# Performance work log

Measured on AMD Instinct MI355X. Metric: run time of the kernel, lower is better.

## Reference

```python
import jax, jax.numpy as jnp
import numpy as np

N_NODES = 40000
N_EDGES = 1280000
D_FEAT = 1024
HIDDEN = 64
N_CLASSES = 40


def gcn_conv(x, edge_index, W, b):
    # PyG GCNConv: linear transform, add self-loops, symmetric deg^{-1/2} normalization, scatter-add
    n = x.shape[0]
    h = x @ W  # [N, out]
    loop = jnp.arange(n, dtype=edge_index.dtype)
    row = jnp.concatenate([edge_index[0], loop])  # source
    col = jnp.concatenate([edge_index[1], loop])  # target
    deg = jax.ops.segment_sum(jnp.ones_like(col, dtype=x.dtype), col, num_segments=n)
    dinv = jnp.where(deg > 0, jax.lax.rsqrt(deg), 0.0).astype(x.dtype)
    norm = dinv[row] * dinv[col]  # [E+N]
    msg = h[row] * norm[:, None]
    out = jax.ops.segment_sum(msg, col, num_segments=n)
    return out + b


def setup_inputs() -> dict:
    key = jax.random.key(0)
    k1, k2, k3, k4 = jax.random.split(key, 4)
    x = jax.random.normal(k1, (N_NODES, D_FEAT), dtype=jnp.float32)
    edge_index = jax.random.randint(k2, (2, N_EDGES), 0, N_NODES, dtype=jnp.int32)
    W1 = jax.random.normal(k3, (D_FEAT, HIDDEN), dtype=jnp.float32) * (1.0 / np.sqrt(D_FEAT))
    b1 = jnp.zeros((HIDDEN,), dtype=jnp.float32)
    W2 = jax.random.normal(k4, (HIDDEN, N_CLASSES), dtype=jnp.float32) * (1.0 / np.sqrt(HIDDEN))
    b2 = jnp.zeros((N_CLASSES,), dtype=jnp.float32)
    return {"x": x, "edge_index": edge_index, "W1": W1, "b1": b1, "W2": W2, "b2": b2}


def reference(x, edge_index, W1, b1, W2, b2):
    h = gcn_conv(x, edge_index, W1, b1)
    h = jax.nn.relu(h)
    # F.dropout(training=False) -> identity in eval mode
    h = gcn_conv(h, edge_index, W2, b2)
    return jax.nn.log_softmax(h, axis=1)
```

## Files before the change

### kernel.cpp

```cpp
#include <hip/hip_runtime.h>
#include <hip/hip_bf16.h>
#include <math.h>

#define N_NODES 40000
#define N_EDGES 1280000
#define D_FEAT 1024
#define HIDDEN 64
#define N_CLASSES 40
#define NB 157
#define CHUNK 2048
#define SORT_STAGE 10240

typedef _Float16 f16x8 __attribute__((ext_vector_type(8)));
typedef float f32x4 __attribute__((ext_vector_type(4)));

__device__ __forceinline__ int wscan64(int v, int lane) {
#pragma unroll
    for (int d = 1; d < 64; d <<= 1) {
        int t = __shfl_up(v, d, 64);
        v += (lane >= d) ? t : 0;
    }
    return v;
}


#define HIST_BLOCKS 313
#define CONV_BLOCKS 256

__global__ __launch_bounds__(256) void k_pre(const int* __restrict__ col,
                                             int* __restrict__ btot,
                                             const float* __restrict__ W,
                                             _Float16* __restrict__ Wt) {
    __shared__ int h[NB];
    int tid = threadIdx.x;
    if (blockIdx.x < HIST_BLOCKS) {
        if (tid < NB) h[tid] = 0;
        __syncthreads();
        int e0 = blockIdx.x * 4096;
#pragma unroll
        for (int t = 0; t < 4; ++t) {
            int e = e0 + t * 1024 + tid * 4;
            if (e < N_EDGES) {
                int4 c = *(const int4*)&col[e];
                atomicAdd(&h[c.x >> 8], 1);
                atomicAdd(&h[c.y >> 8], 1);
                atomicAdd(&h[c.z >> 8], 1);
                atomicAdd(&h[c.w >> 8], 1);
            }
        }
        __syncthreads();
        if (tid < NB && h[tid]) atomicAdd(&btot[tid], h[tid]);
    } else {
        int i = (blockIdx.x - HIST_BLOCKS) * 256 + tid;
        int n = i & 63, k = i >> 6;
        Wt[n * D_FEAT + k] = (_Float16)W[k * HIDDEN + n];
    }
}


__global__ __launch_bounds__(256) void k_scanbb(const int* __restrict__ btot,
                                                int* __restrict__ bb) {
    __shared__ int wsum[4];
    const int tid = threadIdx.x;
    const int wave = tid >> 6, lane = tid & 63;
    int v = (tid < NB) ? btot[tid] : 0;
    int iv = wscan64(v, lane);
    if (lane == 63) wsum[wave] = iv;
    __syncthreads();
    int add = 0;
#pragma unroll
    for (int w = 0; w < 3; ++w)
        add += (w < wave) ? wsum[w] : 0;
    if (tid < NB) bb[tid] = iv + add - v;
}


__global__ __launch_bounds__(256) void k_binscatter(const int* __restrict__ row,
                                                    const int* __restrict__ col,
                                                    const int* __restrict__ bb,
                                                    int* __restrict__ gcur,
                                                    unsigned* __restrict__ sedge) {
    __shared__ unsigned stage[CHUNK];
    __shared__ unsigned char bo[CHUNK];
    __shared__ int hist[NB];
    __shared__ int lo[NB];
    __shared__ int cur[NB];
    __shared__ int dst[NB];
    __shared__ int wsum[4];
    const int tid = threadIdx.x;
    const int wave = tid >> 6, lane = tid & 63;
    const int e0 = blockIdx.x * CHUNK;

    if (tid < NB) { hist[tid] = 0; cur[tid] = 0; }
    __syncthreads();

    int c[8];
#pragma unroll
    for (int t = 0; t < 8; ++t) {
        int e = tid + t * 256;
        c[t] = col[e0 + e];
        atomicAdd(&hist[c[t] >> 8], 1);
    }
    __syncthreads();

    int hv = (tid < NB) ? hist[tid] : 0;
    int iv = wscan64(hv, lane);
    if (lane == 63) wsum[wave] = iv;
    __syncthreads();
    int add = 0;
#pragma unroll
    for (int w = 0; w < 3; ++w)
        add += (w < wave) ? wsum[w] : 0;
    if (tid < NB) {
        int excl = iv + add - hv;
        lo[tid] = excl;
        int cp = hv ? atomicAdd(&gcur[tid], hv) : 0;
        dst[tid] = bb[tid] + cp - excl;
    }
    __syncthreads();

#pragma unroll
    for (int t = 0; t < 8; ++t) {
        int e = tid + t * 256;
        int b = c[t] >> 8;
        int p = lo[b] + atomicAdd(&cur[b], 1);
        stage[p] = ((unsigned)(c[t] & 255) << 16) | (unsigned)row[e0 + e];
        bo[p] = (unsigned char)b;
    }
    __syncthreads();
    for (int i = tid; i < CHUNK; i += 256)
        sedge[dst[bo[i]] + i] = stage[i];
}


__global__ __launch_bounds__(512) void k_bucketsort(const unsigned* __restrict__ sedge,
                                                    const int* __restrict__ btot,
                                                    const int* __restrict__ bb,
                                                    int* __restrict__ off,
                                                    float* __restrict__ dinv,
                                                    unsigned short* __restrict__ sorted) {
    __shared__ int hist[256];
    __shared__ int cur[256];
    __shared__ unsigned short st[SORT_STAGE];
    __shared__ int wsum[4];
    const int tid = threadIdx.x;
    const int wave = tid >> 6, lane = tid & 63;
    const int b = blockIdx.x;
    const int base = bb[b];
    const int cnt  = btot[b];
    const int end  = base + cnt;

    if (tid < 256) hist[tid] = 0;
    __syncthreads();

    for (int i = base + tid; i < end; i += 512)
        atomicAdd(&hist[sedge[i] >> 16], 1);
    __syncthreads();

    int v = 0, iv = 0;
    if (tid < 256) {
        v = hist[tid];
        iv = wscan64(v, lane);
        if (lane == 63) wsum[wave] = iv;
    }
    __syncthreads();
    if (tid < 256) {
        int add = 0;
#pragma unroll
        for (int w = 0; w < 3; ++w)
            add += (w < wave) ? wsum[w] : 0;
        int excl = iv + add - v;
        cur[tid] = excl;
        int col0 = b << 8;
        int ncol = min(256, N_NODES - col0);
        if (tid < ncol) {
            off[col0 + tid] = base + excl;
            dinv[col0 + tid] = rsqrtf((float)(v + 1));
        }
    }
    if (b == NB - 1 && tid == 0) off[N_NODES] = N_EDGES;
    __syncthreads();

    if (cnt <= SORT_STAGE) {
        for (int i = base + tid; i < end; i += 512) {
            unsigned e = sedge[i];
            int p = atomicAdd(&cur[e >> 16], 1);
            st[p] = (unsigned short)e;
        }
        __syncthreads();
        for (int i = tid; i < cnt; i += 512)
            sorted[base + i] = st[i];
    } else {
        for (int i = base + tid; i < end; i += 512) {
            unsigned e = sedge[i];
            int p = atomicAdd(&cur[e >> 16], 1);
            sorted[base + p] = (unsigned short)e;
        }
    }
}


#define LDA 72
#define LDB 72

__global__ __launch_bounds__(256) void k_gemm1(const float* __restrict__ X,
                                               const _Float16* __restrict__ Wt,
                                               const float* __restrict__ dinv,
                                               _Float16* __restrict__ out) {
    __shared__ _Float16 As[2][64 * LDA];
    __shared__ _Float16 Bs[2][64 * LDB];
    const int tid = threadIdx.x;
    const int wave = tid >> 6, lane = tid & 63;
    const int row0 = blockIdx.x * 64;
    const int m0 = (wave & 1) * 32, n0 = (wave >> 1) * 32;
    const int lr = lane & 15, quad = lane >> 4;

    const int ar = tid >> 2;
    const int ak = (tid & 3) * 16;
    const int bn = tid >> 2;
    const int bk = (tid & 3) * 16;

    f32x4 acc00 = {0.f,0.f,0.f,0.f}, acc01 = {0.f,0.f,0.f,0.f};
    f32x4 acc10 = {0.f,0.f,0.f,0.f}, acc11 = {0.f,0.f,0.f,0.f};

    float4 xv0, xv1, xv2, xv3;
    uint4 wv0, wv1;

#define GLOAD(K0) {                                                          \
        const float4* xp = (const float4*)&X[(row0 + ar) * D_FEAT + (K0) + ak]; \
        xv0 = xp[0]; xv1 = xp[1]; xv2 = xp[2]; xv3 = xp[3];                  \
        const uint4* wp = (const uint4*)&Wt[bn * D_FEAT + (K0) + bk];        \
        wv0 = wp[0]; wv1 = wp[1]; }

#define LSTORE(B) {                                                          \
        f16x8 p0 = {(_Float16)xv0.x,(_Float16)xv0.y,(_Float16)xv0.z,(_Float16)xv0.w, \
                    (_Float16)xv1.x,(_Float16)xv1.y,(_Float16)xv1.z,(_Float16)xv1.w}; \
        f16x8 p1 = {(_Float16)xv2.x,(_Float16)xv2.y,(_Float16)xv2.z,(_Float16)xv2.w, \
                    (_Float16)xv3.x,(_Float16)xv3.y,(_Float16)xv3.z,(_Float16)xv3.w}; \
        *(f16x8*)&As[B][ar * LDA + ak]     = p0;                             \
        *(f16x8*)&As[B][ar * LDA + ak + 8] = p1;                             \
        *(uint4*)&Bs[B][bn * LDB + bk]     = wv0;                            \
        *(uint4*)&Bs[B][bn * LDB + bk + 8] = wv1; }

#define MFMA_STEP(B) {                                                       \
        _Pragma("unroll")                                                    \
        for (int kk = 0; kk < 64; kk += 32) {                                \
            f16x8 a0 = *(f16x8*)&As[B][(m0 + lr) * LDA + kk + quad * 8];     \
            f16x8 a1 = *(f16x8*)&As[B][(m0 + 16 + lr) * LDA + kk + quad * 8];\
            f16x8 b0 = *(f16x8*)&Bs[B][(n0 + lr) * LDB + kk + quad * 8];     \
            f16x8 b1 = *(f16x8*)&Bs[B][(n0 + 16 + lr) * LDB + kk + quad * 8];\
            acc00 = __builtin_amdgcn_mfma_f32_16x16x32_f16(a0, b0, acc00, 0, 0, 0); \
            acc01 = __builtin_amdgcn_mfma_f32_16x16x32_f16(a0, b1, acc01, 0, 0, 0); \
            acc10 = __builtin_amdgcn_mfma_f32_16x16x32_f16(a1, b0, acc10, 0, 0, 0); \
            acc11 = __builtin_amdgcn_mfma_f32_16x16x32_f16(a1, b1, acc11, 0, 0, 0); \
        } }

    GLOAD(0);
    LSTORE(0);
    __syncthreads();
    int buf = 0;
    for (int k0 = 64; k0 < D_FEAT; k0 += 64) {
        GLOAD(k0);
        MFMA_STEP(buf);
        LSTORE(buf ^ 1);
        __syncthreads();
        buf ^= 1;
    }
    MFMA_STEP(buf);

#pragma unroll
    for (int r = 0; r < 4; ++r) {
        int m = row0 + m0 + quad * 4 + r;
        float dv0 = dinv[m], dv1 = dinv[m + 16];
        out[m * HIDDEN + n0 + lr]             = (_Float16)(acc00[r] * dv0);
        out[m * HIDDEN + n0 + 16 + lr]        = (_Float16)(acc01[r] * dv0);
        out[(m + 16) * HIDDEN + n0 + lr]      = (_Float16)(acc10[r] * dv1);
        out[(m + 16) * HIDDEN + n0 + 16 + lr] = (_Float16)(acc11[r] * dv1);
    }
#undef GLOAD
#undef LSTORE
#undef MFMA_STEP
}


__global__ __launch_bounds__(256) void k_agg1(const int* __restrict__ off,
                                              const unsigned short* __restrict__ sorted,
                                              const _Float16* __restrict__ hs,
                                              const float* __restrict__ dinv,
                                              const float* __restrict__ bias,
                                              _Float16* __restrict__ A1) {
    const int tid = threadIdx.x;
    const int wave = tid >> 6, lane = tid & 63;
    const int node = blockIdx.x * 4 + wave;
    const int g = lane >> 3;
    const int sl = lane & 7;

    float acc[8];
#pragma unroll
    for (int j = 0; j < 8; ++j) acc[j] = 0.f;
    if (g == 0) {
        f16x8 v = *(const f16x8*)&hs[node * HIDDEN + sl * 8];
#pragma unroll
        for (int j = 0; j < 8; ++j) acc[j] = (float)v[j];
    }

    const int beg = off[node], end = off[node + 1];
    for (int base = beg; base < end; base += 64) {
        int m = end - base; if (m > 64) m = 64;
        int vidx = (lane < m) ? (int)sorted[base + lane] : 0;
        int nfull = m & ~15;
        int i = 0;
        for (; i < nfull; i += 16) {
            int s0 = __shfl(vidx, i + g, 64);
            int s1 = __shfl(vidx, i + 8 + g, 64);
            f16x8 v0 = *(const f16x8*)&hs[s0 * HIDDEN + sl * 8];
            f16x8 v1 = *(const f16x8*)&hs[s1 * HIDDEN + sl * 8];
            f16x8 t = v0 + v1;
#pragma unroll
            for (int j = 0; j < 8; ++j)
                acc[j] += (float)t[j];
        }
        if (i < m) {
            int s0 = __shfl(vidx, i + g, 64);
            int s1 = __shfl(vidx, i + 8 + g, 64);
            f16x8 v0 = {};
            f16x8 v1 = {};
            if (i + g < m)     v0 = *(const f16x8*)&hs[s0 * HIDDEN + sl * 8];
            if (i + 8 + g < m) v1 = *(const f16x8*)&hs[s1 * HIDDEN + sl * 8];
            f16x8 t = v0 + v1;
#pragma unroll
            for (int j = 0; j < 8; ++j)
                acc[j] += (float)t[j];
        }
    }

#pragma unroll
    for (int j = 0; j < 8; ++j) {
        acc[j] += __shfl_xor(acc[j], 8, 64);
        acc[j] += __shfl_xor(acc[j], 16, 64);
        acc[j] += __shfl_xor(acc[j], 32, 64);
    }
    if (lane < 8) {
        float dv = dinv[node];
        f16x8 o;
#pragma unroll
        for (int j = 0; j < 8; ++j) {
            float z = fmaf(dv, acc[j], bias[lane * 8 + j]);
            o[j] = (_Float16)(fmaxf(z, 0.f) * dv);
        }
        *(f16x8*)&A1[node * HIDDEN + lane * 8] = o;
    }
}


__global__ __launch_bounds__(256) void k_agg2_lsm(const int* __restrict__ off,
                                                  const unsigned short* __restrict__ sorted,
                                                  const _Float16* __restrict__ A1,
                                                  const float* __restrict__ dinv,
                                                  const float* __restrict__ b2,
                                                  const float* __restrict__ W2,
                                                  float* __restrict__ out) {
    __shared__ float W2s[HIDDEN * N_CLASSES];
    __shared__ float aggs[4][HIDDEN];
    const int tid = threadIdx.x;
    for (int i = tid; i < HIDDEN * N_CLASSES; i += 256) W2s[i] = W2[i];
    const int wave = tid >> 6, lane = tid & 63;
    const int node = blockIdx.x * 4 + wave;
    const int g = lane >> 3, sl = lane & 7;

    float acc[8];
#pragma unroll
    for (int j = 0; j < 8; ++j) acc[j] = 0.f;
    if (g == 0) {
        f16x8 v = *(const f16x8*)&A1[node * HIDDEN + sl * 8];
#pragma unroll
        for (int j = 0; j < 8; ++j) acc[j] = (float)v[j];
    }
    __syncthreads();

    const int beg = off[node], end = off[node + 1];
    for (int base = beg; base < end; base += 64) {
        int m = end - base; if (m > 64) m = 64;
        int vidx = (lane < m) ? (int)sorted[base + lane] : 0;
        int nfull = m & ~15;
        int i = 0;
        for (; i < nfull; i += 16) {
            int s0 = __shfl(vidx, i + g, 64);
            int s1 = __shfl(vidx, i + 8 + g, 64);
            f16x8 v0 = *(const f16x8*)&A1[s0 * HIDDEN + sl * 8];
            f16x8 v1 = *(const f16x8*)&A1[s1 * HIDDEN + sl * 8];
            f16x8 t = v0 + v1;
#pragma unroll
            for (int j = 0; j < 8; ++j)
                acc[j] += (float)t[j];
        }
        if (i < m) {
            int s0 = __shfl(vidx, i + g, 64);
            int s1 = __shfl(vidx, i + 8 + g, 64);
            f16x8 v0 = {};
            f16x8 v1 = {};
            if (i + g < m)     v0 = *(const f16x8*)&A1[s0 * HIDDEN + sl * 8];
            if (i + 8 + g < m) v1 = *(const f16x8*)&A1[s1 * HIDDEN + sl * 8];
            f16x8 t = v0 + v1;
#pragma unroll
            for (int j = 0; j < 8; ++j)
                acc[j] += (float)t[j];
        }
    }
#pragma unroll
    for (int j = 0; j < 8; ++j) {
        acc[j] += __shfl_xor(acc[j], 8, 64);
        acc[j] += __shfl_xor(acc[j], 16, 64);
        acc[j] += __shfl_xor(acc[j], 32, 64);
    }
    if (lane < 8) {
        f32x4 t0 = {acc[0], acc[1], acc[2], acc[3]};
        f32x4 t1 = {acc[4], acc[5], acc[6], acc[7]};
        *(f32x4*)&aggs[wave][lane * 8]     = t0;
        *(f32x4*)&aggs[wave][lane * 8 + 4] = t1;
    }
    __builtin_amdgcn_wave_barrier();

    float z = -INFINITY;
    if (lane < N_CLASSES) {
        float s = 0.f;
        const float* ag = aggs[wave];
#pragma unroll
        for (int k = 0; k < HIDDEN; ++k)
            s = fmaf(ag[k], W2s[k * N_CLASSES + lane], s);
        z = fmaf(dinv[node], s, b2[lane]);
    }
    float mv = z;
#pragma unroll
    for (int d = 32; d > 0; d >>= 1) mv = fmaxf(mv, __shfl_xor(mv, d, 64));
    float ex = (lane < N_CLASSES) ? expf(z - mv) : 0.f;
#pragma unroll
    for (int d = 32; d > 0; d >>= 1) ex += __shfl_xor(ex, d, 64);
    float lse = mv + logf(ex);
    if (lane < N_CLASSES) out[node * N_CLASSES + lane] = z - lse;
}


extern "C" void kernel_launch(void* const* d_in, const int* in_sizes, int n_in,
                              void* d_out, int out_size, void* d_ws, size_t ws_size,
                              hipStream_t stream) {
    const float* x  = (const float*)d_in[0];
    const int*   ei = (const int*)d_in[1];
    const float* W1 = (const float*)d_in[2];
    const float* b1 = (const float*)d_in[3];
    const float* W2 = (const float*)d_in[4];
    const float* b2 = (const float*)d_in[5];
    const int* row = ei;
    const int* col = ei + N_EDGES;

    char* ws = (char*)d_ws;
    int*            btot   = (int*)(ws + 0);
    int*            gcur   = (int*)(ws + 1024);
    int*            bb     = (int*)(ws + 2048);
    int*            off    = (int*)(ws + 4096);
    float*          dinv   = (float*)(ws + 167936);
    unsigned*       sedge  = (unsigned*)(ws + 335872);
    unsigned short* sorted = (unsigned short*)(ws + 5455872);
    _Float16*       W1t    = (_Float16*)(ws + 8015872);
    _Float16*       B1     = (_Float16*)(ws + 8146944);
    _Float16*       A1     = (_Float16*)(ws + 335872);

    hipMemsetAsync(btot, 0, 2048, stream);
    k_pre<<<HIST_BLOCKS + CONV_BLOCKS, 256, 0, stream>>>(col, btot, W1, W1t);
    k_scanbb<<<1, 256, 0, stream>>>(btot, bb);
    k_binscatter<<<N_EDGES / CHUNK, 256, 0, stream>>>(row, col, bb, gcur, sedge);
    k_bucketsort<<<NB, 512, 0, stream>>>(sedge, btot, bb, off, dinv, sorted);

    k_gemm1<<<N_NODES / 64, 256, 0, stream>>>(x, W1t, dinv, B1);
    k_agg1<<<N_NODES / 4, 256, 0, stream>>>(off, sorted, B1, dinv, b1, A1);
    k_agg2_lsm<<<N_NODES / 4, 256, 0, stream>>>(off, sorted, A1, dinv, b2, W2, (float*)d_out);
}
```

Before: 370.3 us.

## Overlap GEMM with edge sort via merged multi-role kernels and move dinv scaling

Drops the separate bucket-offset scan kernel by recomputing the scan inside each binscatter and sort block. Splits the dense X@W1 GEMM across two merged launches, so its blocks run alongside the binscatter and bucket-sort phases instead of after them. Because the GEMM no longer waits for dinv, the source-side normalization moves into agg1, which packs each neighbor's fp16 dinv with its index and scales per edge. This saves launches and hides the sort latency behind GEMM work, at the cost of more shared-memory per block, redundant scans, extra per-edge fp16 multiplies, and some lost precision in the normalization.

```diff
diff --git a/kernel.cpp b/kernel.cpp
--- a/kernel.cpp
+++ b/kernel.cpp
@@ -10,6 +10,9 @@
 #define NB 157
 #define CHUNK 2048
 #define SORT_STAGE 10240
+#define GEMM_BLOCKS 625
+#define GEMM_A 312
+#define GEMM_B 313
 
 typedef _Float16 f16x8 __attribute__((ext_vector_type(8)));
 typedef float f32x4 __attribute__((ext_vector_type(4)));
@@ -58,64 +61,58 @@
 }
 
 
-__global__ __launch_bounds__(256) void k_scanbb(const int* __restrict__ btot,
-                                                int* __restrict__ bb) {
-    __shared__ int wsum[4];
-    const int tid = threadIdx.x;
-    const int wave = tid >> 6, lane = tid & 63;
-    int v = (tid < NB) ? btot[tid] : 0;
-    int iv = wscan64(v, lane);
-    if (lane == 63) wsum[wave] = iv;
-    __syncthreads();
-    int add = 0;
-#pragma unroll
-    for (int w = 0; w < 3; ++w)
-        add += (w < wave) ? wsum[w] : 0;
-    if (tid < NB) bb[tid] = iv + add - v;
-}
-
-
-__global__ __launch_bounds__(256) void k_binscatter(const int* __restrict__ row,
-                                                    const int* __restrict__ col,
-                                                    const int* __restrict__ bb,
-                                                    int* __restrict__ gcur,
-                                                    unsigned* __restrict__ sedge) {
-    __shared__ unsigned stage[CHUNK];
-    __shared__ unsigned char bo[CHUNK];
-    __shared__ int hist[NB];
-    __shared__ int lo[NB];
-    __shared__ int cur[NB];
-    __shared__ int dst[NB];
-    __shared__ int wsum[4];
-    const int tid = threadIdx.x;
-    const int wave = tid >> 6, lane = tid & 63;
-    const int e0 = blockIdx.x * CHUNK;
-
-    if (tid < NB) { hist[tid] = 0; cur[tid] = 0; }
-    __syncthreads();
+struct BinS {
+    unsigned stage[CHUNK];
+    unsigned char bo[CHUNK];
+    int hist[NB]; int lo[NB]; int cur[NB]; int dst[NB];
+    int wsA[4]; int wsB[4];
+};
+struct SortS {
+    int hist[256]; int cur[256];
+    unsigned short st[SORT_STAGE];
+    int ws[4];
+    int sbase, scnt;
+};
+#define GEMM_SMEM 36864
+
+
+__device__ __forceinline__ void binscatter_body(char* smem, int bx,
+        const int* __restrict__ row, const int* __restrict__ col,
+        const int* __restrict__ btot, int* __restrict__ gcur,
+        unsigned* __restrict__ sedge, int tid, int wave, int lane) {
+    BinS* S = (BinS*)smem;
+    const int e0 = bx * CHUNK;
+    if (tid < NB) { S->hist[tid] = 0; S->cur[tid] = 0; }
+    int bv = (tid < NB) ? btot[tid] : 0;
+    int ivb = wscan64(bv, lane);
+    if (lane == 63) S->wsB[wave] = ivb;
+    __syncthreads();
+    int addb = 0;
+#pragma unroll
+    for (int w = 0; w < 3; ++w) addb += (w < wave) ? S->wsB[w] : 0;
+    int bbv = ivb + addb - bv;
 
     int c[8];
 #pragma unroll
     for (int t = 0; t < 8; ++t) {
         int e = tid + t * 256;
         c[t] = col[e0 + e];
-        atomicAdd(&hist[c[t] >> 8], 1);
-    }
-    __syncthreads();
-
-    int hv = (tid < NB) ? hist[tid] : 0;
+        atomicAdd(&S->hist[c[t] >> 8], 1);
+    }
+    __syncthreads();
+
+    int hv = (tid < NB) ? S->hist[tid] : 0;
     int iv = wscan64(hv, lane);
-    if (lane == 63) wsum[wave] = iv;
+    if (lane == 63) S->wsA[wave] = iv;
     __syncthreads();
     int add = 0;
 #pragma unroll
-    for (int w = 0; w < 3; ++w)
-        add += (w < wave) ? wsum[w] : 0;
+    for (int w = 0; w < 3; ++w) add += (w < wave) ? S->wsA[w] : 0;
     if (tid < NB) {
         int excl = iv + add - hv;
-        lo[tid] = excl;
+        S->lo[tid] = excl;
         int cp = hv ? atomicAdd(&gcur[tid], hv) : 0;
-        dst[tid] = bb[tid] + cp - excl;
+        S->dst[tid] = bbv + cp - excl;
     }
     __syncthreads();
 
@@ -123,77 +120,67 @@
     for (int t = 0; t < 8; ++t) {
         int e = tid + t * 256;
         int b = c[t] >> 8;
-        int p = lo[b] + atomicAdd(&cur[b], 1);
-        stage[p] = ((unsigned)(c[t] & 255) << 16) | (unsigned)row[e0 + e];
-        bo[p] = (unsigned char)b;
+        int p = S->lo[b] + atomicAdd(&S->cur[b], 1);
+        S->stage[p] = ((unsigned)(c[t] & 255) << 16) | (unsigned)row[e0 + e];
+        S->bo[p] = (unsigned char)b;
     }
     __syncthreads();
     for (int i = tid; i < CHUNK; i += 256)
-        sedge[dst[bo[i]] + i] = stage[i];
-}
-
-
-__global__ __launch_bounds__(512) void k_bucketsort(const unsigned* __restrict__ sedge,
-                                                    const int* __restrict__ btot,
-                                                    const int* __restrict__ bb,
-                                                    int* __restrict__ off,
-                                                    float* __restrict__ dinv,
-                                                    unsigned short* __restrict__ sorted) {
-    __shared__ int hist[256];
-    __shared__ int cur[256];
-    __shared__ unsigned short st[SORT_STAGE];
-    __shared__ int wsum[4];
-    const int tid = threadIdx.x;
-    const int wave = tid >> 6, lane = tid & 63;
-    const int b = blockIdx.x;
-    const int base = bb[b];
-    const int cnt  = btot[b];
-    const int end  = base + cnt;
-
-    if (tid < 256) hist[tid] = 0;
-    __syncthreads();
-
-    for (int i = base + tid; i < end; i += 512)
-        atomicAdd(&hist[sedge[i] >> 16], 1);
-    __syncthreads();
-
-    int v = 0, iv = 0;
-    if (tid < 256) {
-        v = hist[tid];
-        iv = wscan64(v, lane);
-        if (lane == 63) wsum[wave] = iv;
-    }
-    __syncthreads();
-    if (tid < 256) {
-        int add = 0;
-#pragma unroll
-        for (int w = 0; w < 3; ++w)
-            add += (w < wave) ? wsum[w] : 0;
-        int excl = iv + add - v;
-        cur[tid] = excl;
-        int col0 = b << 8;
-        int ncol = min(256, N_NODES - col0);
-        if (tid < ncol) {
-            off[col0 + tid] = base + excl;
-            dinv[col0 + tid] = rsqrtf((float)(v + 1));
-        }
+        sedge[S->dst[S->bo[i]] + i] = S->stage[i];
+}
+
+
+__device__ __forceinline__ void sort_body(char* smem, int b,
+        const unsigned* __restrict__ sedge, const int* __restrict__ btot,
+        int* __restrict__ off, float* __restrict__ dinv,
+        unsigned short* __restrict__ sorted, int tid, int wave, int lane) {
+    SortS* S = (SortS*)smem;
+    S->hist[tid] = 0;
+    int bv = (tid < NB) ? btot[tid] : 0;
+    int ivb = wscan64(bv, lane);
+    if (lane == 63) S->ws[wave] = ivb;
+    __syncthreads();
+    int addb = 0;
+#pragma unroll
+    for (int w = 0; w < 3; ++w) addb += (w < wave) ? S->ws[w] : 0;
+    if (tid == b) { S->sbase = ivb + addb - bv; S->scnt = bv; }
+    __syncthreads();
+    const int base = S->sbase, cnt = S->scnt, end = base + cnt;
+
+    for (int i = base + tid; i < end; i += 256)
+        atomicAdd(&S->hist[sedge[i] >> 16], 1);
+    __syncthreads();
+    int v = S->hist[tid];
+    int iv = wscan64(v, lane);
+    if (lane == 63) S->ws[wave] = iv;
+    __syncthreads();
+    int add = 0;
+#pragma unroll
+    for (int w = 0; w < 3; ++w) add += (w < wave) ? S->ws[w] : 0;
+    int excl = iv + add - v;
+    S->cur[tid] = excl;
+    int col0 = b << 8;
+    int ncol = min(256, N_NODES - col0);
+    if (tid < ncol) {
+        off[col0 + tid] = base + excl;
+        dinv[col0 + tid] = rsqrtf((float)(v + 1));
     }
     if (b == NB - 1 && tid == 0) off[N_NODES] = N_EDGES;
     __syncthreads();
 
     if (cnt <= SORT_STAGE) {
-        for (int i = base + tid; i < end; i += 512) {
+        for (int i = base + tid; i < end; i += 256) {
             unsigned e = sedge[i];
-            int p = atomicAdd(&cur[e >> 16], 1);
-            st[p] = (unsigned short)e;
+            int p = atomicAdd(&S->cur[e >> 16], 1);
+            S->st[p] = (unsigned short)e;
         }
         __syncthreads();
-        for (int i = tid; i < cnt; i += 512)
-            sorted[base + i] = st[i];
+        for (int i = tid; i < cnt; i += 256)
+            sorted[base + i] = S->st[i];
     } else {
-        for (int i = base + tid; i < end; i += 512) {
+        for (int i = base + tid; i < end; i += 256) {
             unsigned e = sedge[i];
-            int p = atomicAdd(&cur[e >> 16], 1);
+            int p = atomicAdd(&S->cur[e >> 16], 1);
             sorted[base + p] = (unsigned short)e;
         }
     }
@@ -203,15 +190,13 @@
 #define LDA 72
 #define LDB 72
 
-__global__ __launch_bounds__(256) void k_gemm1(const float* __restrict__ X,
-                                               const _Float16* __restrict__ Wt,
-                                               const float* __restrict__ dinv,
-                                               _Float16* __restrict__ out) {
-    __shared__ _Float16 As[2][64 * LDA];
-    __shared__ _Float16 Bs[2][64 * LDB];
-    const int tid = threadIdx.x;
+__device__ __forceinline__ void gemm_body(char* smem, int bx,
+        const float* __restrict__ X, const _Float16* __restrict__ Wt,
+        _Float16* __restrict__ out, int tid) {
+    auto As = (_Float16(*)[64 * LDA])(smem);
+    auto Bs = (_Float16(*)[64 * LDB])(smem + 2 * 64 * LDA * 2);
     const int wave = tid >> 6, lane = tid & 63;
-    const int row0 = blockIdx.x * 64;
+    const int row0 = bx * 64;
     const int m0 = (wave & 1) * 32, n0 = (wave >> 1) * 32;
     const int lr = lane & 15, quad = lane >> 4;
 
@@ -271,15 +256,39 @@
 #pragma unroll
     for (int r = 0; r < 4; ++r) {
         int m = row0 + m0 + quad * 4 + r;
-        float dv0 = dinv[m], dv1 = dinv[m + 16];
-        out[m * HIDDEN + n0 + lr]             = (_Float16)(acc00[r] * dv0);
-        out[m * HIDDEN + n0 + 16 + lr]        = (_Float16)(acc01[r] * dv0);
-        out[(m + 16) * HIDDEN + n0 + lr]      = (_Float16)(acc10[r] * dv1);
-        out[(m + 16) * HIDDEN + n0 + 16 + lr] = (_Float16)(acc11[r] * dv1);
+        out[m * HIDDEN + n0 + lr]             = (_Float16)acc00[r];
+        out[m * HIDDEN + n0 + 16 + lr]        = (_Float16)acc01[r];
+        out[(m + 16) * HIDDEN + n0 + lr]      = (_Float16)acc10[r];
+        out[(m + 16) * HIDDEN + n0 + 16 + lr] = (_Float16)acc11[r];
     }
 #undef GLOAD
 #undef LSTORE
 #undef MFMA_STEP
+}
+
+
+__global__ __launch_bounds__(256) void k_mix(int phase,
+        const int* __restrict__ row, const int* __restrict__ col,
+        const int* __restrict__ btot, int* __restrict__ gcur,
+        unsigned* __restrict__ sedge,
+        int* __restrict__ off, float* __restrict__ dinv,
+        unsigned short* __restrict__ sorted,
+        const float* __restrict__ X, const _Float16* __restrict__ Wt,
+        _Float16* __restrict__ B1) {
+    __shared__ __align__(16) char smem[GEMM_SMEM];
+    const int tid = threadIdx.x;
+    const int wave = tid >> 6, lane = tid & 63;
+    if (phase == 0) {
+        if (blockIdx.x < 625)
+            binscatter_body(smem, blockIdx.x, row, col, btot, gcur, sedge, tid, wave, lane);
+        else
+            gemm_body(smem, (int)blockIdx.x - 625, X, Wt, B1, tid);
+    } else {
+        if (blockIdx.x < NB)
+            sort_body(smem, blockIdx.x, sedge, btot, off, dinv, sorted, tid, wave, lane);
+        else
+            gemm_body(smem, (int)blockIdx.x - NB + GEMM_A, X, Wt, B1, tid);
+    }
 }
 
 
@@ -299,35 +308,49 @@
 #pragma unroll
     for (int j = 0; j < 8; ++j) acc[j] = 0.f;
     if (g == 0) {
+        float dvn = dinv[node];
         f16x8 v = *(const f16x8*)&hs[node * HIDDEN + sl * 8];
 #pragma unroll
-        for (int j = 0; j < 8; ++j) acc[j] = (float)v[j];
+        for (int j = 0; j < 8; ++j) acc[j] = (float)v[j] * dvn;
     }
 
     const int beg = off[node], end = off[node + 1];
     for (int base = beg; base < end; base += 64) {
         int m = end - base; if (m > 64) m = 64;
-        int vidx = (lane < m) ? (int)sorted[base + lane] : 0;
+        unsigned pk = 0;
+        if (lane < m) {
+            int vv = (int)sorted[base + lane];
+            _Float16 dvh = (_Float16)dinv[vv];
+            pk = (unsigned)vv | ((unsigned)__builtin_bit_cast(unsigned short, dvh) << 16);
+        }
         int nfull = m & ~15;
         int i = 0;
         for (; i < nfull; i += 16) {
-            int s0 = __shfl(vidx, i + g, 64);
-            int s1 = __shfl(vidx, i + 8 + g, 64);
-            f16x8 v0 = *(const f16x8*)&hs[s0 * HIDDEN + sl * 8];
-            f16x8 v1 = *(const f16x8*)&hs[s1 * HIDDEN + sl * 8];
-            f16x8 t = v0 + v1;
+            unsigned p0 = (unsigned)__shfl((int)pk, i + g, 64);
+            unsigned p1 = (unsigned)__shfl((int)pk, i + 8 + g, 64);
+            const f16x8 v0 = *(const f16x8*)&hs[(p0 & 0xffffu) * HIDDEN + sl * 8];
+            const f16x8 v1 = *(const f16x8*)&hs[(p1 & 0xffffu) * HIDDEN + sl * 8];
+            _Float16 d0 = __builtin_bit_cast(_Float16, (unsigned short)(p0 >> 16));
+            _Float16 d1 = __builtin_bit_cast(_Float16, (unsigned short)(p1 >> 16));
+            f16x8 t = v0 * d0 + v1 * d1;
 #pragma unroll
             for (int j = 0; j < 8; ++j)
                 acc[j] += (float)t[j];
         }
         if (i < m) {
-            int s0 = __shfl(vidx, i + g, 64);
-            int s1 = __shfl(vidx, i + 8 + g, 64);
-            f16x8 v0 = {};
-            f16x8 v1 = {};
-            if (i + g < m)     v0 = *(const f16x8*)&hs[s0 * HIDDEN + sl * 8];
-            if (i + 8 + g < m) v1 = *(const f16x8*)&hs[s1 * HIDDEN + sl * 8];
-            f16x8 t = v0 + v1;
+            unsigned p0 = (unsigned)__shfl((int)pk, i + g, 64);
+            unsigned p1 = (unsigned)__shfl((int)pk, i + 8 + g, 64);
+            f16x8 v0 = {}, v1 = {};
+            _Float16 d0 = (_Float16)0.f, d1 = (_Float16)0.f;
+            if (i + g < m) {
+                v0 = *(const f16x8*)&hs[(p0 & 0xffffu) * HIDDEN + sl * 8];
+                d0 = __builtin_bit_cast(_Float16, (unsigned short)(p0 >> 16));
+            }
+            if (i + 8 + g < m) {
+                v1 = *(const f16x8*)&hs[(p1 & 0xffffu) * HIDDEN + sl * 8];
+                d1 = __builtin_bit_cast(_Float16, (unsigned short)(p1 >> 16));
+            }
+            f16x8 t = v0 * d0 + v1 * d1;
 #pragma unroll
             for (int j = 0; j < 8; ++j)
                 acc[j] += (float)t[j];
@@ -456,7 +479,6 @@
     char* ws = (char*)d_ws;
     int*            btot   = (int*)(ws + 0);
     int*            gcur   = (int*)(ws + 1024);
-    int*            bb     = (int*)(ws + 2048);
     int*            off    = (int*)(ws + 4096);
     float*          dinv   = (float*)(ws + 167936);
     unsigned*       sedge  = (unsigned*)(ws + 335872);
@@ -467,11 +489,10 @@
 
     hipMemsetAsync(btot, 0, 2048, stream);
     k_pre<<<HIST_BLOCKS + CONV_BLOCKS, 256, 0, stream>>>(col, btot, W1, W1t);
-    k_scanbb<<<1, 256, 0, stream>>>(btot, bb);
-    k_binscatter<<<N_EDGES / CHUNK, 256, 0, stream>>>(row, col, bb, gcur, sedge);
-    k_bucketsort<<<NB, 512, 0, stream>>>(sedge, btot, bb, off, dinv, sorted);
-
-    k_gemm1<<<N_NODES / 64, 256, 0, stream>>>(x, W1t, dinv, B1);
+    k_mix<<<625 + GEMM_A, 256, 0, stream>>>(0, row, col, btot, gcur, sedge,
+                                            off, dinv, sorted, x, W1t, B1);
+    k_mix<<<NB + GEMM_B, 256, 0, stream>>>(1, row, col, btot, gcur, sedge,
+                                           off, dinv, sorted, x, W1t, B1);
     k_agg1<<<N_NODES / 4, 256, 0, stream>>>(off, sorted, B1, dinv, b1, A1);
     k_agg2_lsm<<<N_NODES / 4, 256, 0, stream>>>(off, sorted, A1, dinv, b2, W2, (float*)d_out);
 }
```

New measurement: 355.7 us. -4.0%, faster.
